# Performance work log

Hardware: AMD Instinct MI355X
Metric: run time of the kernel (lower is better)

Reference implementation:

```python
import jax, jax.numpy as jnp
import numpy as np
from math import exp

C1 = 0.01 ** 2
C2 = 0.03 ** 2
WINDOW_SIZE = 11
SIGMA = 1.5

def make_window(window_size, channel, sigma=SIGMA):
    g = np.array([exp(-(x - window_size // 2) ** 2 / float(2 * sigma ** 2))
                  for x in range(window_size)], dtype=np.float32)
    g = g / g.sum()
    w2d = np.outer(g, g).astype(np.float32)  # [ws, ws]
    # depthwise kernel, OIHW with I=1 per group: [C, 1, ws, ws]
    return jnp.asarray(np.broadcast_to(w2d, (channel, 1, window_size, window_size)).copy())

def depthwise_conv(x, window, pad):
    C = x.shape[1]
    return jax.lax.conv_general_dilated(
        x, window, window_strides=(1, 1),
        padding=[(pad, pad), (pad, pad)],
        feature_group_count=C,
        dimension_numbers=('NCHW', 'OIHW', 'NCHW'))

def setup_inputs() -> dict:
    key = jax.random.key(0)
    k1, k2 = jax.random.split(key)
    B, C, H, W = 16, 3, 512, 512
    img1 = jax.random.uniform(k1, (B, C, H, W), dtype=jnp.float32)
    img2 = jax.random.uniform(k2, (B, C, H, W), dtype=jnp.float32)
    window = make_window(WINDOW_SIZE, C)
    return {"img1": img1, "img2": img2, "window": window}

def reference(img1, img2, window):
    pad = WINDOW_SIZE // 2
    mu1 = depthwise_conv(img1, window, pad)
    mu2 = depthwise_conv(img2, window, pad)
    mu1_sq = mu1 * mu1
    mu2_sq = mu2 * mu2
    mu1_mu2 = mu1 * mu2
    sigma1_sq = depthwise_conv(img1 * img1, window, pad) - mu1_sq
    sigma2_sq = depthwise_conv(img2 * img2, window, pad) - mu2_sq
    sigma12 = depthwise_conv(img1 * img2, window, pad) - mu1_mu2
    ssim_cs = (2 * sigma12 + C2) / (sigma1_sq + sigma2_sq + C2)
    ssim_l = (2 * mu1_mu2 + C1) / (mu1_sq + mu2_sq + C1)
    ssim_map = ssim_l * ssim_cs
    return jnp.mean(ssim_map)
```

## Files before the change

### kernel.cpp

```cpp
#include <hip/hip_runtime.h>


typedef float v2f __attribute__((ext_vector_type(2)));

#define IMG_H 512
#define IMG_W 512
#define N_IMG 48
#define WS 11
#define PAD 5
#define CHUNK 16
#define NCHUNK (IMG_H / CHUNK)
#define RING 12
#define PLANE_B 4736
#define INV_NPX (1.0f / (48.0f * 512.0f * 512.0f))

__device__ __forceinline__ unsigned swz(int E) { return 8u * E + 8u * (E >> 3); }

__device__ __forceinline__ v2f vfma(v2f a, v2f b, v2f c) {
    return __builtin_elementwise_fma(a, b, c);
}

__global__ __launch_bounds__(256) void ssim_partial_kernel(
    const float* __restrict__ img1,
    const float* __restrict__ img2,
    const float* __restrict__ window,
    float* __restrict__ out)
{
    __shared__ __align__(16) char lds[4 * PLANE_B];
    __shared__ float wred[4];
#define LDSE(p, off) (*(v2f*)(lds + (p) * PLANE_B + (off)))

    const int tid = threadIdx.x;
    const int bc  = blockIdx.x;
    const int r0  = blockIdx.y * CHUNK;
    const int col = tid * 2;

    float g[WS];
    {
        const float g5  = sqrtf(window[5 * WS + 5]);
        const float inv = 1.0f / g5;
#pragma unroll
        for (int j = 0; j < WS; ++j) g[j] = window[5 * WS + j] * inv;
    }
    const float C1v = 0.01f * 0.01f;
    const float C2v = 0.03f * 0.03f;

    const float* __restrict__ p1 = img1 + (size_t)bc * (IMG_H * IMG_W);
    const float* __restrict__ p2 = img2 + (size_t)bc * (IMG_H * IMG_W);

    unsigned roff[12];
#pragma unroll
    for (int m = 0; m < 12; ++m) roff[m] = swz(2 * tid + 1 + m);
    const unsigned woffA = swz(2 * tid + 6);
    const unsigned woffB = swz(2 * tid + 7);

    for (int i = tid; i < 48; i += 256) {
        const int p = i / 12, h = i % 12;
        const int E = (h < 6) ? h : (512 + h);
        LDSE(p, swz(E)) = (v2f)(0.0f);
    }
    __syncthreads();

    v2f rx1[RING], rx2[RING];
#pragma unroll
    for (int i = 0; i < RING; ++i) { rx1[i] = (v2f)(0.0f); rx2[i] = (v2f)(0.0f); }

#pragma unroll
    for (int i = 0; i < 10; ++i) {
        const int rr = r0 - PAD + i;
        v2f u1 = (v2f)(0.0f), u2 = (v2f)(0.0f);
        if (rr >= 0 && rr < IMG_H) {
            u1 = *(const v2f*)(p1 + rr * IMG_W + col);
            u2 = *(const v2f*)(p2 + rr * IMG_W + col);
        }
        rx1[2 + i] = u1; rx2[2 + i] = u2;
    }

    float acc = 0.0f;

    for (int step = 0; step < CHUNK / 2; ++step) {
        const int R = r0 + step * 2;

#pragma unroll
        for (int i = 0; i < RING - 2; ++i) { rx1[i] = rx1[i + 2]; rx2[i] = rx2[i + 2]; }
#pragma unroll
        for (int j = 0; j < 2; ++j) {
            const int rr = R + PAD + j;
            v2f u1 = (v2f)(0.0f), u2 = (v2f)(0.0f);
            if (rr < IMG_H) {
                u1 = *(const v2f*)(p1 + rr * IMG_W + col);
                u2 = *(const v2f*)(p2 + rr * IMG_W + col);
            }
            rx1[10 + j] = u1; rx2[10 + j] = u2;
        }

        v2f a1_0 = (v2f)(0.f), a2_0 = (v2f)(0.f), aS_0 = (v2f)(0.f), aP_0 = (v2f)(0.f);
        v2f a1_1 = (v2f)(0.f), a2_1 = (v2f)(0.f), aS_1 = (v2f)(0.f), aP_1 = (v2f)(0.f);
#pragma unroll
        for (int i = 0; i < WS; ++i) {
            const float w = g[i];
            {
                const v2f X1 = rx1[i], X2 = rx2[i];
                a1_0 = vfma((v2f)(w), X1, a1_0);
                a2_0 = vfma((v2f)(w), X2, a2_0);
                aS_0 = vfma((v2f)(w), vfma(X1, X1, X2 * X2), aS_0);
                aP_0 = vfma((v2f)(w), X1 * X2, aP_0);
            }
            {
                const v2f X1 = rx1[i + 1], X2 = rx2[i + 1];
                a1_1 = vfma((v2f)(w), X1, a1_1);
                a2_1 = vfma((v2f)(w), X2, a2_1);
                aS_1 = vfma((v2f)(w), vfma(X1, X1, X2 * X2), aS_1);
                aP_1 = vfma((v2f)(w), X1 * X2, aP_1);
            }
        }
        LDSE(0, woffA) = (v2f){a1_0.x, a1_1.x}; LDSE(0, woffB) = (v2f){a1_0.y, a1_1.y};
        LDSE(1, woffA) = (v2f){a2_0.x, a2_1.x}; LDSE(1, woffB) = (v2f){a2_0.y, a2_1.y};
        LDSE(2, woffA) = (v2f){aS_0.x, aS_1.x}; LDSE(2, woffB) = (v2f){aS_0.y, aS_1.y};
        LDSE(3, woffA) = (v2f){aP_0.x, aP_1.x}; LDSE(3, woffB) = (v2f){aP_0.y, aP_1.y};
        __syncthreads();

        v2f hA[4], hB[4];
#pragma unroll
        for (int p = 0; p < 4; ++p) {
            v2f r[12];
#pragma unroll
            for (int m = 0; m < 12; ++m) r[m] = LDSE(p, roff[m]);
            v2f sA = (v2f)(0.f), sB = (v2f)(0.f);
#pragma unroll
            for (int i = 0; i < WS; ++i) {
                sA = vfma((v2f)(g[i]), r[i],     sA);
                sB = vfma((v2f)(g[i]), r[i + 1], sB);
            }
            hA[p] = sA; hB[p] = sB;
        }
#pragma unroll
        for (int k = 0; k < 2; ++k) {
            const v2f mu1 = k ? hB[0] : hA[0];
            const v2f mu2 = k ? hB[1] : hA[1];
            const v2f hs  = k ? hB[2] : hA[2];
            const v2f hp  = k ? hB[3] : hA[3];
            const v2f mu1s = mu1 * mu1;
            const v2f mu2s = mu2 * mu2;
            const v2f mu12 = mu1 * mu2;
            const v2f sgs  = hs - mu1s - mu2s;
            const v2f sg12 = hp - mu12;
            const v2f num  = (2.f * mu12 + (v2f)(C1v)) * (2.f * sg12 + (v2f)(C2v));
            const v2f den  = (mu1s + mu2s + (v2f)(C1v)) * (sgs + (v2f)(C2v));
            v2f r = {__builtin_amdgcn_rcpf(den.x), __builtin_amdgcn_rcpf(den.y)};
            r = r * vfma(-den, r, (v2f)(2.0f));
            acc = fmaf(num.x, r.x, acc);
            acc = fmaf(num.y, r.y, acc);
        }
        __syncthreads();
    }

#pragma unroll
    for (int off = 32; off > 0; off >>= 1)
        acc += __shfl_down(acc, off);
    if ((tid & 63) == 0) wred[tid >> 6] = acc;
    __syncthreads();
    if (tid == 0) {
        const float s = (wred[0] + wred[1]) + (wred[2] + wred[3]);
        atomicAdd(out, s * INV_NPX);
    }
}

extern "C" void kernel_launch(void* const* d_in, const int* in_sizes, int n_in,
                              void* d_out, int out_size, void* d_ws, size_t ws_size,
                              hipStream_t stream) {
    const float* img1   = (const float*)d_in[0];
    const float* img2   = (const float*)d_in[1];
    const float* window = (const float*)d_in[2];
    float* out = (float*)d_out;

    hipMemsetAsync(out, 0, sizeof(float), stream);
    dim3 grid(N_IMG, NCHUNK);
    ssim_partial_kernel<<<grid, 256, 0, stream>>>(img1, img2, window, out);
}
```

Measured before the change: 146.6 us.

## Process four rows per step with a new LDS layout and XOR swizzle

Each step of the SSIM kernel now handles four output rows instead of two. The vertical pass computes four row-pairs per thread into two LDS plane sets. In the horizontal pass, half the threads each take one row pair and compute four adjacent columns from 14 loaded values, so fewer LDS loads are spent per output. The padded swizzle is replaced by an XOR swizzle that shrinks each plane, and launch bounds request 3 blocks per CU. The aim is fewer barriers and less LDS traffic per output, at the cost of more registers and a doubled LDS footprint.

After: 142.0 us. 1.03x faster.

```diff
diff --git a/kernel.cpp b/kernel.cpp
--- a/kernel.cpp
+++ b/kernel.cpp
@@ -10,25 +10,25 @@
 #define PAD 5
 #define CHUNK 16
 #define NCHUNK (IMG_H / CHUNK)
-#define RING 12
-#define PLANE_B 4736
+#define RING 14
+#define PLANE_B 4224
 #define INV_NPX (1.0f / (48.0f * 512.0f * 512.0f))
 
-__device__ __forceinline__ unsigned swz(int E) { return 8u * E + 8u * (E >> 3); }
-
+__device__ __forceinline__ unsigned swz8(int E) {
+    return (unsigned)((E ^ (((E >> 4) & 7) << 1)) * 8);
+}
 __device__ __forceinline__ v2f vfma(v2f a, v2f b, v2f c) {
     return __builtin_elementwise_fma(a, b, c);
 }
 
-__global__ __launch_bounds__(256) void ssim_partial_kernel(
+__global__ __launch_bounds__(256, 3) void ssim_partial_kernel(
     const float* __restrict__ img1,
     const float* __restrict__ img2,
     const float* __restrict__ window,
     float* __restrict__ out)
 {
-    __shared__ __align__(16) char lds[4 * PLANE_B];
+    __shared__ __align__(16) char lds[8 * PLANE_B];
     __shared__ float wred[4];
-#define LDSE(p, off) (*(v2f*)(lds + (p) * PLANE_B + (off)))
 
     const int tid = threadIdx.x;
     const int bc  = blockIdx.x;
@@ -48,16 +48,18 @@
     const float* __restrict__ p1 = img1 + (size_t)bc * (IMG_H * IMG_W);
     const float* __restrict__ p2 = img2 + (size_t)bc * (IMG_H * IMG_W);
 
-    unsigned roff[12];
+    const unsigned woffA = swz8(col + 6);
+    const unsigned woffB = swz8(col + 7);
+    const int q  = tid & 127;
+    const int jj = tid >> 7;
+    unsigned roff[14];
 #pragma unroll
-    for (int m = 0; m < 12; ++m) roff[m] = swz(2 * tid + 1 + m);
-    const unsigned woffA = swz(2 * tid + 6);
-    const unsigned woffB = swz(2 * tid + 7);
+    for (int m = 0; m < 14; ++m) roff[m] = swz8(4 * q + 1 + m);
 
-    for (int i = tid; i < 48; i += 256) {
-        const int p = i / 12, h = i % 12;
-        const int E = (h < 6) ? h : (512 + h);
-        LDSE(p, swz(E)) = (v2f)(0.0f);
+    if (tid < 96) {
+        const int pj = tid / 12, h = tid % 12;
+        const int E  = (h < 6) ? h : (512 + h);
+        *(v2f*)(lds + pj * PLANE_B + swz8(E)) = (v2f)(0.0f);
     }
     __syncthreads();
 
@@ -73,18 +75,18 @@
             u1 = *(const v2f*)(p1 + rr * IMG_W + col);
             u2 = *(const v2f*)(p2 + rr * IMG_W + col);
         }
-        rx1[2 + i] = u1; rx2[2 + i] = u2;
+        rx1[4 + i] = u1; rx2[4 + i] = u2;
     }
 
     float acc = 0.0f;
 
-    for (int step = 0; step < CHUNK / 2; ++step) {
-        const int R = r0 + step * 2;
+    for (int step = 0; step < CHUNK / 4; ++step) {
+        const int R = r0 + step * 4;
 
 #pragma unroll
-        for (int i = 0; i < RING - 2; ++i) { rx1[i] = rx1[i + 2]; rx2[i] = rx2[i + 2]; }
+        for (int i = 0; i < RING - 4; ++i) { rx1[i] = rx1[i + 4]; rx2[i] = rx2[i + 4]; }
 #pragma unroll
-        for (int j = 0; j < 2; ++j) {
+        for (int j = 0; j < 4; ++j) {
             const int rr = R + PAD + j;
             v2f u1 = (v2f)(0.0f), u2 = (v2f)(0.0f);
             if (rr < IMG_H) {
@@ -94,52 +96,53 @@
             rx1[10 + j] = u1; rx2[10 + j] = u2;
         }
 
-        v2f a1_0 = (v2f)(0.f), a2_0 = (v2f)(0.f), aS_0 = (v2f)(0.f), aP_0 = (v2f)(0.f);
-        v2f a1_1 = (v2f)(0.f), a2_1 = (v2f)(0.f), aS_1 = (v2f)(0.f), aP_1 = (v2f)(0.f);
+        v2f va[4][4];
 #pragma unroll
-        for (int i = 0; i < WS; ++i) {
-            const float w = g[i];
-            {
-                const v2f X1 = rx1[i], X2 = rx2[i];
-                a1_0 = vfma((v2f)(w), X1, a1_0);
-                a2_0 = vfma((v2f)(w), X2, a2_0);
-                aS_0 = vfma((v2f)(w), vfma(X1, X1, X2 * X2), aS_0);
-                aP_0 = vfma((v2f)(w), X1 * X2, aP_0);
-            }
-            {
-                const v2f X1 = rx1[i + 1], X2 = rx2[i + 1];
-                a1_1 = vfma((v2f)(w), X1, a1_1);
-                a2_1 = vfma((v2f)(w), X2, a2_1);
-                aS_1 = vfma((v2f)(w), vfma(X1, X1, X2 * X2), aS_1);
-                aP_1 = vfma((v2f)(w), X1 * X2, aP_1);
+        for (int p = 0; p < 4; ++p)
+#pragma unroll
+            for (int k = 0; k < 4; ++k) va[p][k] = (v2f)(0.0f);
+#pragma unroll
+        for (int k = 0; k < 4; ++k) {
+#pragma unroll
+            for (int i = 0; i < WS; ++i) {
+                const v2f w  = (v2f)(g[i]);
+                const v2f X1 = rx1[i + k], X2 = rx2[i + k];
+                va[0][k] = vfma(w, X1, va[0][k]);
+                va[1][k] = vfma(w, X2, va[1][k]);
+                va[2][k] = vfma(w, vfma(X1, X1, X2 * X2), va[2][k]);
+                va[3][k] = vfma(w, X1 * X2, va[3][k]);
             }
         }
-        LDSE(0, woffA) = (v2f){a1_0.x, a1_1.x}; LDSE(0, woffB) = (v2f){a1_0.y, a1_1.y};
-        LDSE(1, woffA) = (v2f){a2_0.x, a2_1.x}; LDSE(1, woffB) = (v2f){a2_0.y, a2_1.y};
-        LDSE(2, woffA) = (v2f){aS_0.x, aS_1.x}; LDSE(2, woffB) = (v2f){aS_0.y, aS_1.y};
-        LDSE(3, woffA) = (v2f){aP_0.x, aP_1.x}; LDSE(3, woffB) = (v2f){aP_0.y, aP_1.y};
+#pragma unroll
+        for (int jp = 0; jp < 2; ++jp) {
+#pragma unroll
+            for (int p = 0; p < 4; ++p) {
+                char* base = lds + (jp * 4 + p) * PLANE_B;
+                *(v2f*)(base + woffA) = (v2f){va[p][2 * jp].x, va[p][2 * jp + 1].x};
+                *(v2f*)(base + woffB) = (v2f){va[p][2 * jp].y, va[p][2 * jp + 1].y};
+            }
+        }
         __syncthreads();
 
-        v2f hA[4], hB[4];
+        v2f h[4][4];
 #pragma unroll
         for (int p = 0; p < 4; ++p) {
-            v2f r[12];
+            const char* base = lds + (jj * 4 + p) * PLANE_B;
+            v2f r[14];
 #pragma unroll
-            for (int m = 0; m < 12; ++m) r[m] = LDSE(p, roff[m]);
-            v2f sA = (v2f)(0.f), sB = (v2f)(0.f);
+            for (int m = 0; m < 14; ++m) r[m] = *(const v2f*)(base + roff[m]);
 #pragma unroll
-            for (int i = 0; i < WS; ++i) {
-                sA = vfma((v2f)(g[i]), r[i],     sA);
-                sB = vfma((v2f)(g[i]), r[i + 1], sB);
+            for (int d = 0; d < 4; ++d) {
+                v2f s = (v2f)(0.0f);
+#pragma unroll
+                for (int i = 0; i < WS; ++i) s = vfma((v2f)(g[i]), r[d + i], s);
+                h[p][d] = s;
             }
-            hA[p] = sA; hB[p] = sB;
         }
 #pragma unroll
-        for (int k = 0; k < 2; ++k) {
-            const v2f mu1 = k ? hB[0] : hA[0];
-            const v2f mu2 = k ? hB[1] : hA[1];
-            const v2f hs  = k ? hB[2] : hA[2];
-            const v2f hp  = k ? hB[3] : hA[3];
+        for (int d = 0; d < 4; ++d) {
+            const v2f mu1 = h[0][d], mu2 = h[1][d];
+            const v2f hs  = h[2][d], hp  = h[3][d];
             const v2f mu1s = mu1 * mu1;
             const v2f mu2s = mu2 * mu2;
             const v2f mu12 = mu1 * mu2;
```
